# Optimization experiments

Measured on AMD Instinct MI355X. Metric: run time of the kernel, lower is better.

The kernel has to match this reference:

```python
import jax, jax.numpy as jnp
import numpy as np

B, S = 2, 2048
HID, NH, NKV, HD = 1024, 16, 4, 64
E, TOPK, INTER = 8, 2, 2816
WIN = 64
EPS = 1e-8
AUX = 0.01
NREP = NH // NKV


def _rmsnorm(x, w):
    xf = x.astype(jnp.float32)
    var = jnp.mean(xf * xf, axis=-1, keepdims=True)
    return (w * (xf * jax.lax.rsqrt(var + EPS))).astype(x.dtype)


def _rope(x, cos, sin):
    # x: [B,S,H,HD]; cos/sin: [1,S,HD//2]; matches torch view_as_complex on (..,-1,2) pairs
    xr, xi = x[..., 0::2], x[..., 1::2]
    c = cos[:, :, None, :]
    s = sin[:, :, None, :]
    return jnp.stack([xr * c - xi * s, xr * s + xi * c], axis=-1).reshape(x.shape)


def setup_inputs():
    key = jax.random.key(0)
    ks = jax.random.split(key, 12)
    sc = 0.02
    hidden_state = jax.random.normal(ks[0], (B, S, HID), jnp.float32)
    attention_mask = jnp.ones((B, S), jnp.int32)
    inv = 1.0 / (10000.0 ** (np.arange(0, HD, 2, dtype=np.float32) / HD))
    ang = np.outer(np.arange(S, dtype=np.float32), inv)
    freqs_cos = jnp.asarray(np.cos(ang), jnp.float32)[None]
    freqs_sin = jnp.asarray(np.sin(ang), jnp.float32)[None]
    wq = jax.random.normal(ks[1], (HID, NH * HD), jnp.float32) * sc
    wk = jax.random.normal(ks[2], (HID, NKV * HD), jnp.float32) * sc
    wv = jax.random.normal(ks[3], (HID, NKV * HD), jnp.float32) * sc
    wo = jax.random.normal(ks[4], (NH * HD, HID), jnp.float32) * sc
    router_w = jax.random.normal(ks[5], (HID, E), jnp.float32) * sc
    gate_w = jax.random.normal(ks[6], (E, HID, INTER), jnp.float32) * sc
    up_w = jax.random.normal(ks[7], (E, HID, INTER), jnp.float32) * sc
    down_w = jax.random.normal(ks[8], (E, INTER, HID), jnp.float32) * sc
    norm1_w = jnp.ones((HID,), jnp.float32)
    norm2_w = jnp.ones((HID,), jnp.float32)
    return dict(hidden_state=hidden_state, freqs_cos=freqs_cos, freqs_sin=freqs_sin,
                wq=wq, wk=wk, wv=wv, wo=wo, router_w=router_w,
                gate_w=gate_w, up_w=up_w, down_w=down_w,
                norm1_w=norm1_w, norm2_w=norm2_w, attention_mask=attention_mask)


def _attention(x, freqs_cos, freqs_sin, attention_mask, wq, wk, wv, wo):
    b, s, _ = x.shape
    q = (x @ wq).reshape(b, s, NH, HD)
    k = (x @ wk).reshape(b, s, NKV, HD)
    v = (x @ wv).reshape(b, s, NKV, HD)
    q = _rope(q, freqs_cos, freqs_sin)
    k = _rope(k, freqs_cos, freqs_sin)
    k = jnp.repeat(k, NREP, axis=2)  # GQA repeat_kv
    v = jnp.repeat(v, NREP, axis=2)
    scores = jnp.einsum('bqhd,bkhd->bhqk', q, k) / np.float32(np.sqrt(HD))  # [B,H,S,S]
    pos = jnp.arange(s)
    dist = pos[None, :] - pos[:, None]  # j - i
    banned = (dist > 0) | (dist < -WIN)  # causal + sliding window of 64
    scores = jnp.where(banned[None, None], -jnp.inf, scores)
    scores = jnp.where(attention_mask[:, None, None, :] == 0, -jnp.inf, scores)
    scores = jnp.maximum(scores, -1e9)  # matches clamp(min=-1e9)
    probs = jax.nn.softmax(scores.astype(jnp.float32), axis=-1).astype(q.dtype)
    probs = jnp.nan_to_num(probs)
    out = jnp.einsum('bhqk,bkhd->bqhd', probs, v).reshape(b, s, NH * HD)
    return out @ wo


def _moe(x, router_w, gate_w, up_w, down_w):
    b, s, h = x.shape
    xf = x.reshape(-1, h)  # [T, H]
    probs = jax.nn.softmax(xf @ router_w, axis=-1)  # [T, E]
    vals, idx = jax.lax.top_k(probs, TOPK)
    vals = vals / (jnp.sum(vals, axis=-1, keepdims=True) + 1e-9)
    expert_prob = jnp.mean(probs, axis=0)
    load = jnp.mean(jnp.sum(jax.nn.one_hot(idx, E, dtype=jnp.float32), axis=1), axis=0)
    router_loss = E * jnp.sum(expert_prob * load) * AUX
    out = jnp.zeros_like(xf)
    for i in range(E):  # small fixed expert loop; zero-weight tokens contribute nothing
        w_i = jnp.sum(jnp.where(idx == i, vals, 0.0), axis=-1)  # [T]
        h_i = jax.nn.silu(xf @ gate_w[i]) * (xf @ up_w[i])
        out = out + (h_i @ down_w[i]) * w_i[:, None]
    return out.reshape(b, s, h), router_loss


def reference(hidden_state, freqs_cos, freqs_sin, wq, wk, wv, wo,
              router_w, gate_w, up_w, down_w, norm1_w, norm2_w, attention_mask):
    res = hidden_state
    h = _rmsnorm(hidden_state, norm1_w)
    h = _attention(h, freqs_cos, freqs_sin, attention_mask, wq, wk, wv, wo) + res
    res = h
    h2 = _rmsnorm(h, norm2_w)
    moe_out, router_loss = _moe(h2, router_w, gate_w, up_w, down_w)
    return res + moe_out, router_loss
```

## Files before the change

kernel.cpp:

```cpp
#include <hip/hip_runtime.h>
#include <hip/hip_bf16.h>
#include <math.h>

typedef short s16x8 __attribute__((ext_vector_type(8)));
typedef float f32x4 __attribute__((ext_vector_type(4)));
typedef __hip_bfloat16 bf16;

#define NTOK 4096
#define S_LEN 2048
#define HID_C 1024
#define E_C 8
#define INTER_C 2816
#define WIN_C 64
#define CAP 4096
#define NQKV 1536
#define K2C 2048
#define ATILE 16
#define KR 80
#define OUT0_N ((size_t)NTOK*HID_C)

#define AS1 __attribute__((address_space(1)))
#define AS3 __attribute__((address_space(3)))

static __device__ __forceinline__ void gload16(const void* g, void* l){
    __builtin_amdgcn_global_load_lds((AS1 void*)(g), (AS3 void*)(l), 16, 0, 0);
}

static __device__ __forceinline__ float b2f(bf16 v){ return __bfloat162float(v); }
static __device__ __forceinline__ bf16  f2b(float v){ return __float2bfloat16(v); }
static __device__ __forceinline__ short f2bs(float v){ bf16 h = __float2bfloat16(v); return *reinterpret_cast<short*>(&h); }
struct SplitBF { short hi; short lo; };
static __device__ __forceinline__ SplitBF splitf(float x){
    SplitBF r;
    bf16 bh = __float2bfloat16(x);
    r.hi = *reinterpret_cast<short*>(&bh);
    float rem = x - __bfloat162float(bh);
    bf16 bl = __float2bfloat16(rem);
    r.lo = *reinterpret_cast<short*>(&bl);
    return r;
}


__global__ __launch_bounds__(256) void tsplit2s_k(const float* __restrict__ src,
                                                  short* __restrict__ dst,
                                                  int N, int row_off){
    __shared__ float tile[32][33];
    const int n0 = blockIdx.x*32, k0 = blockIdx.y*32;
    const int tx = threadIdx.x & 31, ty = threadIdx.x >> 5;
    #pragma unroll
    for (int i = 0; i < 4; ++i)
        tile[ty + i*8][tx] = src[(size_t)(k0 + ty + i*8)*N + n0 + tx];
    __syncthreads();
    const int g = k0 >> 5;
    const int chH = tx >> 3, chL = 4 | (tx >> 3), off = tx & 7;
    #pragma unroll
    for (int i = 0; i < 4; ++i){
        int nn = ty + i*8;
        SplitBF s = splitf(tile[tx][nn]);
        size_t rowb = (size_t)(row_off + n0 + nn)*K2C + g*64;
        dst[rowb + ((chH ^ ty)<<3) + off] = s.hi;
        dst[rowb + ((chL ^ ty)<<3) + off] = s.lo;
    }
}

__global__ __launch_bounds__(256) void tbf16s_k(const float* __restrict__ src0,
                                                short* __restrict__ dst0, int K, int N){
    const int e = blockIdx.z;
    const float* src = src0 + (size_t)e*K*N;
    short* dst = dst0 + (size_t)e*N*K;
    __shared__ float tile[32][33];
    const int n0 = blockIdx.x*32, k0 = blockIdx.y*32;
    const int tx = threadIdx.x & 31, ty = threadIdx.x >> 5;
    #pragma unroll
    for (int i = 0; i < 4; ++i)
        tile[ty + i*8][tx] = src[(size_t)(k0 + ty + i*8)*N + n0 + tx];
    __syncthreads();
    const int grp  = k0 >> 6;
    const int half = (k0 & 32) >> 3;
    const int ch   = half + (tx >> 3), off = tx & 7;
    #pragma unroll
    for (int i = 0; i < 4; ++i){
        int nn = ty + i*8;
        dst[(size_t)(n0 + nn)*K + grp*64 + ((ch ^ ty)<<3) + off] = f2bs(tile[tx][nn]);
    }
}

__global__ __launch_bounds__(256) void rmsn1c_k(const float* __restrict__ xin,
                                                const float* __restrict__ w,
                                                short* __restrict__ oc){
    const int t = blockIdx.x, tid = threadIdx.x;
    float4 v = *(const float4*)(xin + (size_t)t*HID_C + tid*4);
    float x[4] = {v.x, v.y, v.z, v.w};
    float s = x[0]*x[0]+x[1]*x[1]+x[2]*x[2]+x[3]*x[3];
    #pragma unroll
    for (int off=32; off; off>>=1) s += __shfl_xor(s, off);
    __shared__ float red[4];
    if ((tid&63)==0) red[tid>>6] = s;
    __syncthreads();
    float tot = red[0]+red[1]+red[2]+red[3];
    float sc = rsqrtf(tot*(1.0f/HID_C) + 1e-8f);
    float4 wv = *(const float4*)(w + tid*4);
    float o[4] = { x[0]*sc*wv.x, x[1]*sc*wv.y, x[2]*sc*wv.z, x[3]*sc*wv.w };
    __align__(8) short th[4], tl[4];
    #pragma unroll
    for (int i=0;i<4;++i){ SplitBF sp = splitf(o[i]); th[i]=sp.hi; tl[i]=sp.lo; }
    const int g = tid>>3, q = tid&7;
    const int ch = q>>1, sub = (q&1)*4, key = t&7;
    short* rowp = oc + (size_t)t*K2C + g*64;
    *(uint2*)(rowp + ((ch ^ key)<<3) + sub)      = *(uint2*)th;
    *(uint2*)(rowp + (((4|ch) ^ key)<<3) + sub)  = *(uint2*)tl;
}

__global__ __launch_bounds__(256) void rmsn2_k(const float* __restrict__ xin,
                                               const float* __restrict__ w,
                                               float* __restrict__ outf, bf16* __restrict__ outb){
    const int t = blockIdx.x, tid = threadIdx.x;
    float4 v = *(const float4*)(xin + (size_t)t*HID_C + tid*4);
    float x[4] = {v.x, v.y, v.z, v.w};
    float s = x[0]*x[0]+x[1]*x[1]+x[2]*x[2]+x[3]*x[3];
    #pragma unroll
    for (int off=32; off; off>>=1) s += __shfl_xor(s, off);
    __shared__ float red[4];
    if ((tid&63)==0) red[tid>>6] = s;
    __syncthreads();
    float tot = red[0]+red[1]+red[2]+red[3];
    float sc = rsqrtf(tot*(1.0f/HID_C) + 1e-8f);
    float4 wv = *(const float4*)(w + tid*4);
    float o[4] = { x[0]*sc*wv.x, x[1]*sc*wv.y, x[2]*sc*wv.z, x[3]*sc*wv.w };
    *(float4*)(outf + (size_t)t*HID_C + tid*4) = make_float4(o[0],o[1],o[2],o[3]);
    __align__(8) bf16 tmp[4] = { f2b(o[0]), f2b(o[1]), f2b(o[2]), f2b(o[3]) };
    *(uint2*)(outb + (size_t)t*HID_C + tid*4) = *(uint2*)tmp;
}

template<bool RESID>
__global__ __launch_bounds__(256) void sgemm4_k(const short* __restrict__ A2,
                                                const short* __restrict__ B2,
                                                float* __restrict__ C, const float* __restrict__ resid,
                                                int N){
    __shared__ __align__(16) short lA[2][128*64];
    __shared__ __align__(16) short lB[2][128*64];
    const int tid = threadIdx.x;
    const int bm0 = blockIdx.x*128, bn0 = blockIdx.y*128;
    const int l = tid & 63, w = tid >> 6, wr = w >> 1, wc = w & 1;
    const int lr = l >> 3, lc8 = (l & 7)*8;
    f32x4 acc[4][4] = {};
    auto STAGE = [&](int buf, int kt){
        #pragma unroll
        for (int j = 0; j < 4; ++j){
            int row = w*32 + j*8 + lr;
            gload16(A2 + (size_t)(bm0 + row)*K2C + kt*64 + lc8, &lA[buf][(w*32 + j*8)*64]);
            gload16(B2 + (size_t)(bn0 + row)*K2C + kt*64 + lc8, &lB[buf][(w*32 + j*8)*64]);
        }
    };
    STAGE(0, 0);
    for (int kt = 0; kt < 32; ++kt){
        const int cur = kt & 1;
        if (kt + 1 < 32){
            STAGE(cur ^ 1, kt + 1);
            asm volatile("s_waitcnt vmcnt(8)" ::: "memory");
        } else {
            asm volatile("s_waitcnt vmcnt(0)" ::: "memory");
        }
        __builtin_amdgcn_s_barrier();
        __builtin_amdgcn_sched_barrier(0);
        s16x8 ah[4], al[4], bh[4], bl[4];
        #pragma unroll
        for (int mi = 0; mi < 4; ++mi){
            int r = wr*64 + mi*16 + (l&15);
            int key = r & 7;
            ah[mi] = *(const s16x8*)(&lA[cur][r*64 + (((l>>4) ^ key)<<3)]);
            al[mi] = *(const s16x8*)(&lA[cur][r*64 + (((4|(l>>4)) ^ key)<<3)]);
        }
        #pragma unroll
        for (int ni = 0; ni < 4; ++ni){
            int n = wc*64 + ni*16 + (l&15);
            int key = n & 7;
            bh[ni] = *(const s16x8*)(&lB[cur][n*64 + (((l>>4) ^ key)<<3)]);
            bl[ni] = *(const s16x8*)(&lB[cur][n*64 + (((4|(l>>4)) ^ key)<<3)]);
        }
        #pragma unroll
        for (int mi = 0; mi < 4; ++mi)
            #pragma unroll
            for (int ni = 0; ni < 4; ++ni){
                acc[mi][ni] = __builtin_amdgcn_mfma_f32_16x16x32_bf16(ah[mi], bh[ni], acc[mi][ni], 0,0,0);
                acc[mi][ni] = __builtin_amdgcn_mfma_f32_16x16x32_bf16(ah[mi], bl[ni], acc[mi][ni], 0,0,0);
                acc[mi][ni] = __builtin_amdgcn_mfma_f32_16x16x32_bf16(al[mi], bh[ni], acc[mi][ni], 0,0,0);
            }
        __builtin_amdgcn_s_barrier();
    }
    #pragma unroll
    for (int mi = 0; mi < 4; ++mi)
        #pragma unroll
        for (int ni = 0; ni < 4; ++ni)
            #pragma unroll
            for (int rr = 0; rr < 4; ++rr){
                int row = bm0 + wr*64 + mi*16 + (l>>4)*4 + rr;
                int col = bn0 + wc*64 + ni*16 + (l&15);
                float vv = acc[mi][ni][rr];
                if (RESID) vv += resid[(size_t)row*N + col];
                C[(size_t)row*N + col] = vv;
            }
}

__global__ __launch_bounds__(256) void rope2_k(float* __restrict__ qkv,
                                               const float* __restrict__ cosb, const float* __restrict__ sinb){
    int idx = blockIdx.x*256 + threadIdx.x;
    int t = idx / 640;
    int r = idx - t*640;
    int hs = r >> 5, tp = r & 31;
    int s = t & (S_LEN-1);
    float c  = cosb[s*32+tp];
    float sn = sinb[s*32+tp];
    float* base;
    if (hs < 16) base = qkv + (size_t)t*NQKV + hs*64 + 2*tp;
    else         base = qkv + (size_t)t*NQKV + 1024 + (hs-16)*64 + 2*tp;
    float2 v = *(float2*)base;
    *(float2*)base = make_float2(v.x*c - v.y*sn, v.x*sn + v.y*c);
}

__global__ __launch_bounds__(256) void attn3_k(const float* __restrict__ qkv,
                                               short* __restrict__ oc){
    const int t0 = blockIdx.x * ATILE;
    const int hk = blockIdx.y;
    const int sq0 = t0 & (S_LEN-1);
    const int tokbase = t0 - sq0;
    const int tid = threadIdx.x, l = tid & 63, w = tid >> 6;
    __shared__ float Kl[KR*65];
    __shared__ float Vl[KR*65];
    __shared__ float qsh[4][64];
    __shared__ float ps[4][64];
    for (int rr = tid >> 4; rr < KR; rr += 16){
        int c4 = (tid & 15)*4;
        int kp = sq0 - 64 + rr;
        float4 kv = make_float4(0,0,0,0), vv = kv;
        if (kp >= 0){
            const float* base = qkv + (size_t)(tokbase + kp)*NQKV + 1024 + hk*64 + c4;
            kv = *(const float4*)base;
            vv = *(const float4*)(base + 256);
        }
        Kl[rr*65 + c4+0]=kv.x; Kl[rr*65 + c4+1]=kv.y; Kl[rr*65 + c4+2]=kv.z; Kl[rr*65 + c4+3]=kv.w;
        Vl[rr*65 + c4+0]=vv.x; Vl[rr*65 + c4+1]=vv.y; Vl[rr*65 + c4+2]=vv.z; Vl[rr*65 + c4+3]=vv.w;
    }
    __syncthreads();
    const int h = hk*4 + w;
    for (int i = 0; i < ATILE; ++i){
        const int t = t0 + i, sq = sq0 + i;
        qsh[w][l] = qkv[(size_t)t*NQKV + h*64 + l];
        float d = 0.f;
        const float* krow = &Kl[(i + l)*65];
        #pragma unroll
        for (int c = 0; c < 64; ++c) d += qsh[w][c] * krow[c];
        const bool valid = (sq - 64 + l) >= 0;
        float sc = valid ? d*0.125f : -1e30f;
        float part = qsh[w][l] * Kl[(i + 64)*65 + l];
        #pragma unroll
        for (int off = 32; off; off >>= 1) part += __shfl_xor(part, off);
        float dg = part*0.125f;
        float m = sc;
        #pragma unroll
        for (int off = 32; off; off >>= 1) m = fmaxf(m, __shfl_xor(m, off));
        m = fmaxf(m, dg);
        float e = __expf(sc - m);
        float ssum = e;
        #pragma unroll
        for (int off = 32; off; off >>= 1) ssum += __shfl_xor(ssum, off);
        float edg = __expf(dg - m);
        ssum += edg;
        float inv = 1.f / ssum;
        ps[w][l] = e * inv;
        float pdg = edg * inv;
        float acc = 0.f;
        #pragma unroll 8
        for (int jj = 0; jj < 64; ++jj) acc += ps[w][jj] * Vl[(i + jj)*65 + l];
        acc += pdg * Vl[(i + 64)*65 + l];
        SplitBF sp = splitf(acc);
        const int k = h*64 + l;
        const int g = k>>5, ch = (k&31)>>3, off2 = k&7, key = t&7;
        short* rowp = oc + (size_t)t*K2C + g*64;
        rowp[((ch ^ key)<<3) + off2]     = sp.hi;
        rowp[(((4|ch) ^ key)<<3) + off2] = sp.lo;
    }
}

__global__ __launch_bounds__(256) void router2_k(const float* __restrict__ h2f, const float* __restrict__ rw,
                                                 int* __restrict__ lists, float* __restrict__ wl,
                                                 int* __restrict__ cnt, float* __restrict__ psum){
    const int tid = threadIdx.x, l = tid & 63, w = tid >> 6;
    __shared__ int   sE0[16], sE1[16], sSlot0[16], sSlot1[16];
    __shared__ float sW0[16], sW1[16];
    __shared__ float sPsum[8];
    __shared__ int   sCnt[8], sBase[8];
    if (tid < 8){ sPsum[tid] = 0.f; sCnt[tid] = 0; }
    __syncthreads();
    #pragma unroll
    for (int i = 0; i < 4; ++i){
        const int li = w*4 + i;
        const int t = blockIdx.x*16 + li;
        float lg[8] = {0,0,0,0,0,0,0,0};
        for (int c = 0; c < 16; ++c){
            int kidx = l + c*64;
            float x = h2f[(size_t)t*HID_C + kidx];
            float4 w0 = *(const float4*)(rw + (size_t)kidx*8);
            float4 w1 = *(const float4*)(rw + (size_t)kidx*8 + 4);
            lg[0] += x*w0.x; lg[1] += x*w0.y; lg[2] += x*w0.z; lg[3] += x*w0.w;
            lg[4] += x*w1.x; lg[5] += x*w1.y; lg[6] += x*w1.z; lg[7] += x*w1.w;
        }
        #pragma unroll
        for (int e = 0; e < 8; ++e)
            #pragma unroll
            for (int off=32; off; off>>=1) lg[e] += __shfl_xor(lg[e], off);
        if (l == 0){
            float m = lg[0];
            #pragma unroll
            for (int e = 1; e < 8; ++e) m = fmaxf(m, lg[e]);
            float p[8]; float s = 0.f;
            #pragma unroll
            for (int e = 0; e < 8; ++e){ p[e] = __expf(lg[e]-m); s += p[e]; }
            float invs = 1.f/s;
            #pragma unroll
            for (int e = 0; e < 8; ++e){ p[e] *= invs; atomicAdd(&sPsum[e], p[e]); }
            float best = -1e30f, sec = -1e30f; int bi = 0, si = 0;
            #pragma unroll
            for (int e = 0; e < 8; ++e){
                float pv = p[e];
                if (pv > best){ sec = best; si = bi; best = pv; bi = e; }
                else if (pv > sec){ sec = pv; si = e; }
            }
            float wsum = best + sec + 1e-9f;
            sE0[li] = bi; sE1[li] = si;
            sW0[li] = best/wsum; sW1[li] = sec/wsum;
            sSlot0[li] = atomicAdd(&sCnt[bi], 1);
            sSlot1[li] = atomicAdd(&sCnt[si], 1);
        }
    }
    __syncthreads();
    if (tid < 8){
        sBase[tid] = atomicAdd(&cnt[tid], sCnt[tid]);
        atomicAdd(&psum[tid], sPsum[tid]);
    }
    __syncthreads();
    if (tid < 16){
        int t = blockIdx.x*16 + tid;
        int e0 = sE0[tid], e1 = sE1[tid];
        int s0 = sBase[e0] + sSlot0[tid];
        int s1 = sBase[e1] + sSlot1[tid];
        lists[e0*CAP + s0] = t; wl[e0*CAP + s0] = sW0[tid];
        lists[e1*CAP + s1] = t; wl[e1*CAP + s1] = sW1[tid];
    }
}

__global__ void finalize_k(const int* __restrict__ cnt, const float* __restrict__ psum,
                           int* __restrict__ offs, float* __restrict__ out){
    if (threadIdx.x == 0 && blockIdx.x == 0){
        int o = 0; float loss = 0.f;
        for (int e = 0; e < 8; ++e){
            offs[e] = o; o += cnt[e];
            loss += (psum[e]*(1.0f/NTOK)) * ((float)cnt[e]*(1.0f/NTOK));
        }
        offs[8] = o;
        out[OUT0_N] = loss * (float)E_C * 0.01f;
    }
}

__global__ __launch_bounds__(256) void moe1g3_k(const short* __restrict__ h2b,
                                                const short* __restrict__ gate_t,
                                                const short* __restrict__ up_t,
                                                bf16* __restrict__ inter,
                                                const int* __restrict__ lists,
                                                const int* __restrict__ cnt,
                                                const int* __restrict__ offs){
    const int b = blockIdx.x;
    const int r = b & 7, j = b >> 3;
    const int G = r + ((j >> 5) << 3);
    const int e = G / 44, bnG = G % 44;
    const int bm0 = (j & 31) * 128;
    const int ne = cnt[e];
    if (bm0 >= ne) return;
    const int bn0 = bnG * 64;
    __shared__ __align__(16) short lA[2][128*64];
    __shared__ __align__(16) short lG[2][64*64];
    __shared__ __align__(16) short lU[2][64*64];
    const int tid = threadIdx.x;
    const int l = tid & 63, w = tid >> 6, wr = w >> 1, wc = w & 1;
    const int lr = l >> 3, lc8 = (l & 7)*8;
    const int lcs = (((l & 7) ^ lr) << 3);
    const short* Gb = gate_t + (size_t)e*INTER_C*HID_C;
    const short* Ub = up_t   + (size_t)e*INTER_C*HID_C;
    int tokA[4];
    #pragma unroll
    for (int jj = 0; jj < 4; ++jj){
        int slot = bm0 + w*32 + jj*8 + lr;
        if (slot >= ne) slot = ne - 1;
        tokA[jj] = lists[e*CAP + slot];
    }
    auto STAGE = [&](int buf, int kt){
        #pragma unroll
        for (int jj = 0; jj < 4; ++jj)
            gload16(h2b + (size_t)tokA[jj]*HID_C + kt*64 + lcs, &lA[buf][(w*32 + jj*8)*64]);
        #pragma unroll
        for (int jj = 0; jj < 2; ++jj){
            int n = w*16 + jj*8 + lr;
            gload16(Gb + (size_t)(bn0 + n)*HID_C + kt*64 + lc8, &lG[buf][(w*16 + jj*8)*64]);
            gload16(Ub + (size_t)(bn0 + n)*HID_C + kt*64 + lc8, &lU[buf][(w*16 + jj*8)*64]);
        }
    };
    f32x4 ag[4][2] = {}; f32x4 au[4][2] = {};
    STAGE(0, 0);
    for (int kt = 0; kt < 16; ++kt){
        const int cur = kt & 1;
        if (kt + 1 < 16){
            STAGE(cur ^ 1, kt + 1);
            asm volatile("s_waitcnt vmcnt(8)" ::: "memory");
        } else {
            asm volatile("s_waitcnt vmcnt(0)" ::: "memory");
        }
        __builtin_amdgcn_s_barrier();
        __builtin_amdgcn_sched_barrier(0);
        __builtin_amdgcn_s_setprio(1);
        #pragma unroll
        for (int kk = 0; kk < 64; kk += 32){
            s16x8 af[4], bg[2], bu[2];
            #pragma unroll
            for (int mi = 0; mi < 4; ++mi){
                int ra = wr*64 + mi*16 + (l&15);
                int keyA = ra & 7;
                int chA = (kk>>3) + (l>>4);
                af[mi] = *(const s16x8*)(&lA[cur][ra*64 + ((chA ^ keyA)<<3)]);
            }
            #pragma unroll
            for (int ni = 0; ni < 2; ++ni){
                int n = wc*32 + ni*16 + (l&15);
                int key = n & 7;
                int ch = (kk>>3) + (l>>4);
                bg[ni] = *(const s16x8*)(&lG[cur][n*64 + ((ch ^ key)<<3)]);
                bu[ni] = *(const s16x8*)(&lU[cur][n*64 + ((ch ^ key)<<3)]);
            }
            #pragma unroll
            for (int mi = 0; mi < 4; ++mi)
                #pragma unroll
                for (int ni = 0; ni < 2; ++ni){
                    ag[mi][ni] = __builtin_amdgcn_mfma_f32_16x16x32_bf16(af[mi], bg[ni], ag[mi][ni], 0,0,0);
                    au[mi][ni] = __builtin_amdgcn_mfma_f32_16x16x32_bf16(af[mi], bu[ni], au[mi][ni], 0,0,0);
                }
        }
        __builtin_amdgcn_s_setprio(0);
        __builtin_amdgcn_s_barrier();
    }
    const int obase = offs[e];
    #pragma unroll
    for (int mi = 0; mi < 4; ++mi)
        #pragma unroll
        for (int ni = 0; ni < 2; ++ni)
            #pragma unroll
            for (int rr = 0; rr < 4; ++rr){
                int slot = bm0 + wr*64 + mi*16 + (l>>4)*4 + rr;
                if (slot < ne){
                    int col = bn0 + wc*32 + ni*16 + (l&15);
                    float g = ag[mi][ni][rr], uu = au[mi][ni][rr];
                    float val = (g/(1.f+__expf(-g)))*uu;
                    inter[(size_t)(obase+slot)*INTER_C + col] = f2b(val);
                }
            }
}

__global__ __launch_bounds__(256) void moe2g3_k(const bf16* __restrict__ inter,
                                                const short* __restrict__ down_t,
                                                float* __restrict__ outp,
                                                const float* __restrict__ wl,
                                                const int* __restrict__ lists,
                                                const int* __restrict__ cnt,
                                                const int* __restrict__ offs){
    const int b = blockIdx.x;
    const int r = b & 7, j = b >> 3;
    const int G = r + ((j >> 5) << 3);
    const int e = G >> 3, bnG = G & 7;
    const int bm0 = (j & 31) * 128;
    const int ne = cnt[e];
    if (bm0 >= ne) return;
    const int bn0 = bnG * 128;
    __shared__ __align__(16) short lA[2][128*64];
    __shared__ __align__(16) short lB[2][128*64];
    const int tid = threadIdx.x;
    const int l = tid & 63, w = tid >> 6, wr = w >> 1, wc = w & 1;
    const int lr = l >> 3, lc8 = (l & 7)*8;
    const int lcs = (((l & 7) ^ lr) << 3);
    const int obase = offs[e];
    const short* Db = down_t + (size_t)e*HID_C*INTER_C;
    const short* As = (const short*)inter;
    int rowA[4];
    #pragma unroll
    for (int jj = 0; jj < 4; ++jj){
        int slot = bm0 + w*32 + jj*8 + lr;
        if (slot >= ne) slot = ne - 1;
        rowA[jj] = obase + slot;
    }
    auto STAGE = [&](int buf, int kt){
        #pragma unroll
        for (int jj = 0; jj < 4; ++jj){
            gload16(As + (size_t)rowA[jj]*INTER_C + kt*64 + lcs, &lA[buf][(w*32 + jj*8)*64]);
            int n = w*32 + jj*8 + lr;
            gload16(Db + (size_t)(bn0 + n)*INTER_C + kt*64 + lc8, &lB[buf][(w*32 + jj*8)*64]);
        }
    };
    f32x4 acc[4][4] = {};
    STAGE(0, 0);
    for (int kt = 0; kt < 44; ++kt){
        const int cur = kt & 1;
        if (kt + 1 < 44){
            STAGE(cur ^ 1, kt + 1);
            asm volatile("s_waitcnt vmcnt(8)" ::: "memory");
        } else {
            asm volatile("s_waitcnt vmcnt(0)" ::: "memory");
        }
        __builtin_amdgcn_s_barrier();
        __builtin_amdgcn_sched_barrier(0);
        __builtin_amdgcn_s_setprio(1);
        #pragma unroll
        for (int kk = 0; kk < 64; kk += 32){
            s16x8 af[4], bfr[4];
            #pragma unroll
            for (int mi = 0; mi < 4; ++mi){
                int ra = wr*64 + mi*16 + (l&15);
                int keyA = ra & 7;
                int chA = (kk>>3) + (l>>4);
                af[mi] = *(const s16x8*)(&lA[cur][ra*64 + ((chA ^ keyA)<<3)]);
            }
            #pragma unroll
            for (int ni = 0; ni < 4; ++ni){
                int n = wc*64 + ni*16 + (l&15);
                int key = n & 7;
                int ch = (kk>>3) + (l>>4);
                bfr[ni] = *(const s16x8*)(&lB[cur][n*64 + ((ch ^ key)<<3)]);
            }
            #pragma unroll
            for (int mi = 0; mi < 4; ++mi)
                #pragma unroll
                for (int ni = 0; ni < 4; ++ni)
                    acc[mi][ni] = __builtin_amdgcn_mfma_f32_16x16x32_bf16(af[mi], bfr[ni], acc[mi][ni], 0,0,0);
        }
        __builtin_amdgcn_s_setprio(0);
        __builtin_amdgcn_s_barrier();
    }
    #pragma unroll
    for (int mi = 0; mi < 4; ++mi)
        #pragma unroll
        for (int ni = 0; ni < 4; ++ni)
            #pragma unroll
            for (int rr = 0; rr < 4; ++rr){
                int slot = bm0 + wr*64 + mi*16 + (l>>4)*4 + rr;
                if (slot < ne){
                    int col = bn0 + wc*64 + ni*16 + (l&15);
                    int tok = lists[e*CAP + slot];
                    float wgt = wl[e*CAP + slot];
                    atomicAdd(&outp[(size_t)tok*HID_C + col], acc[mi][ni][rr]*wgt);
                }
            }
}

__global__ __launch_bounds__(256) void final_k(const float* __restrict__ hres,
                                               float* __restrict__ out){
    const int t = blockIdx.x, c = threadIdx.x*4;
    float4 hv = *(const float4*)(hres + (size_t)t*HID_C + c);
    *(float4*)(out + (size_t)t*HID_C + c) = hv;
}

extern "C" void kernel_launch(void* const* d_in, const int* in_sizes, int n_in,
                              void* d_out, int out_size, void* d_ws, size_t ws_size,
                              hipStream_t stream){
    const float* hidden  = (const float*)d_in[0];
    const float* fcos    = (const float*)d_in[1];
    const float* fsin    = (const float*)d_in[2];
    const float* wq      = (const float*)d_in[3];
    const float* wk      = (const float*)d_in[4];
    const float* wv      = (const float*)d_in[5];
    const float* wo      = (const float*)d_in[6];
    const float* routerw = (const float*)d_in[7];
    const float* gatew   = (const float*)d_in[8];
    const float* upw     = (const float*)d_in[9];
    const float* downw   = (const float*)d_in[10];
    const float* n1w     = (const float*)d_in[11];
    const float* n2w     = (const float*)d_in[12];

    char* p = (char*)d_ws;
    size_t off = 0;
    auto alloc = [&](size_t b)->void*{ void* r = p + off; off = (off + b + 255) & ~(size_t)255; return r; };

    int*   cnt    = (int*)alloc(64);
    float* psum   = (float*)alloc(64);
    int*   offs   = (int*)alloc(64);
    int*   lists  = (int*)alloc((size_t)E_C*CAP*4);
    float* wl     = (float*)alloc((size_t)E_C*CAP*4);
    short* wqkv2  = (short*)alloc((size_t)NQKV*K2C*2);
    short* wo2    = (short*)alloc((size_t)HID_C*K2C*2);
    short* gate_t = (short*)alloc((size_t)E_C*INTER_C*HID_C*2);
    short* up_t   = (short*)alloc((size_t)E_C*INTER_C*HID_C*2);
    short* down_t = (short*)alloc((size_t)E_C*HID_C*INTER_C*2);
    short* h1c    = (short*)alloc((size_t)NTOK*K2C*2);
    float* qkvf   = (float*)alloc((size_t)NTOK*NQKV*4);
    float* hres   = (float*)alloc((size_t)NTOK*HID_C*4);
    bf16*  inter  = (bf16*)alloc((size_t)2*NTOK*INTER_C*2);

    short* oc  = h1c;
    float* h2f = qkvf;
    bf16*  h2b = (bf16*)(qkvf + (size_t)NTOK*HID_C);
    float* outp = (float*)d_out;

    (void)hipMemsetAsync(cnt, 0, 64, stream);
    (void)hipMemsetAsync(psum, 0, 64, stream);

    tsplit2s_k<<<dim3(32,32), 256, 0, stream>>>(wq, wqkv2, 1024, 0);
    tsplit2s_k<<<dim3(8,32),  256, 0, stream>>>(wk, wqkv2, 256, 1024);
    tsplit2s_k<<<dim3(8,32),  256, 0, stream>>>(wv, wqkv2, 256, 1280);
    tsplit2s_k<<<dim3(32,32), 256, 0, stream>>>(wo, wo2, 1024, 0);
    tbf16s_k<<<dim3(88,32,8), 256, 0, stream>>>(gatew, gate_t, 1024, 2816);
    tbf16s_k<<<dim3(88,32,8), 256, 0, stream>>>(upw,   up_t,   1024, 2816);
    tbf16s_k<<<dim3(32,88,8), 256, 0, stream>>>(downw, down_t, 2816, 1024);

    rmsn1c_k<<<NTOK, 256, 0, stream>>>(hidden, n1w, h1c);
    sgemm4_k<false><<<dim3(32,12), 256, 0, stream>>>(h1c, wqkv2, qkvf, nullptr, NQKV);
    rope2_k<<<10240, 256, 0, stream>>>(qkvf, fcos, fsin);
    attn3_k<<<dim3(NTOK/ATILE, 4), 256, 0, stream>>>(qkvf, oc);
    sgemm4_k<true><<<dim3(32,8), 256, 0, stream>>>(oc, wo2, hres, hidden, 1024);
    rmsn2_k<<<NTOK, 256, 0, stream>>>(hres, n2w, h2f, h2b);
    router2_k<<<256, 256, 0, stream>>>(h2f, routerw, lists, wl, cnt, psum);
    finalize_k<<<1, 64, 0, stream>>>(cnt, psum, offs, outp);
    final_k<<<NTOK, 256, 0, stream>>>(hres, outp);
    moe1g3_k<<<11264, 256, 0, stream>>>((const short*)h2b, gate_t, up_t, inter, lists, cnt, offs);
    moe2g3_k<<<2048, 256, 0, stream>>>(inter, down_t, outp, wl, lists, cnt, offs);
}
```

Measured before the change: 684.6 us.

## Load MoE weight fragments directly from global into registers, bypassing LDS

Both MoE GEMM kernels now read the B-operand (gate/up and down weights) straight from global memory into MFMA register fragments each k-step, instead of staging them through shared memory. Only the token activations stay double-buffered in LDS. The aim is to cut LDS traffic and footprint, which could raise occupancy and remove LDS reads for B. In exchange, the weight loads are less coalesced (each lane fetches 16 bytes from a different row), they are issued without prefetch ahead of the current step, and tiles shared across waves are fetched redundantly. The vmcnt wait counts are adjusted to match the new number of outstanding loads.

```diff
diff --git a/kernel.cpp b/kernel.cpp
--- a/kernel.cpp
+++ b/kernel.cpp
@@ -362,7 +362,7 @@
     }
 }
 
-__global__ __launch_bounds__(256) void moe1g3_k(const short* __restrict__ h2b,
+__global__ __launch_bounds__(256) void moe1g4_k(const short* __restrict__ h2b,
                                                 const short* __restrict__ gate_t,
                                                 const short* __restrict__ up_t,
                                                 bf16* __restrict__ inter,
@@ -378,11 +378,9 @@
     if (bm0 >= ne) return;
     const int bn0 = bnG * 64;
     __shared__ __align__(16) short lA[2][128*64];
-    __shared__ __align__(16) short lG[2][64*64];
-    __shared__ __align__(16) short lU[2][64*64];
     const int tid = threadIdx.x;
     const int l = tid & 63, w = tid >> 6, wr = w >> 1, wc = w & 1;
-    const int lr = l >> 3, lc8 = (l & 7)*8;
+    const int lr = l >> 3;
     const int lcs = (((l & 7) ^ lr) << 3);
     const short* Gb = gate_t + (size_t)e*INTER_C*HID_C;
     const short* Ub = up_t   + (size_t)e*INTER_C*HID_C;
@@ -393,54 +391,57 @@
         if (slot >= ne) slot = ne - 1;
         tokA[jj] = lists[e*CAP + slot];
     }
+    size_t bOffs[2][2];
+    #pragma unroll
+    for (int kki = 0; kki < 2; ++kki)
+        #pragma unroll
+        for (int ni = 0; ni < 2; ++ni){
+            int n = wc*32 + ni*16 + (l&15);
+            int ch = kki*4 + (l>>4);
+            bOffs[kki][ni] = (size_t)(bn0 + n)*HID_C + (((ch ^ (n&7)))<<3);
+        }
     auto STAGE = [&](int buf, int kt){
         #pragma unroll
         for (int jj = 0; jj < 4; ++jj)
             gload16(h2b + (size_t)tokA[jj]*HID_C + kt*64 + lcs, &lA[buf][(w*32 + jj*8)*64]);
-        #pragma unroll
-        for (int jj = 0; jj < 2; ++jj){
-            int n = w*16 + jj*8 + lr;
-            gload16(Gb + (size_t)(bn0 + n)*HID_C + kt*64 + lc8, &lG[buf][(w*16 + jj*8)*64]);
-            gload16(Ub + (size_t)(bn0 + n)*HID_C + kt*64 + lc8, &lU[buf][(w*16 + jj*8)*64]);
-        }
     };
     f32x4 ag[4][2] = {}; f32x4 au[4][2] = {};
     STAGE(0, 0);
     for (int kt = 0; kt < 16; ++kt){
         const int cur = kt & 1;
+        s16x8 bgv[2][2], buv[2][2];
+        #pragma unroll
+        for (int kki = 0; kki < 2; ++kki)
+            #pragma unroll
+            for (int ni = 0; ni < 2; ++ni){
+                bgv[kki][ni] = *(const s16x8*)(Gb + bOffs[kki][ni] + kt*64);
+                buv[kki][ni] = *(const s16x8*)(Ub + bOffs[kki][ni] + kt*64);
+            }
         if (kt + 1 < 16){
             STAGE(cur ^ 1, kt + 1);
+            asm volatile("s_waitcnt vmcnt(12)" ::: "memory");
+        } else {
             asm volatile("s_waitcnt vmcnt(8)" ::: "memory");
-        } else {
-            asm volatile("s_waitcnt vmcnt(0)" ::: "memory");
         }
         __builtin_amdgcn_s_barrier();
         __builtin_amdgcn_sched_barrier(0);
         __builtin_amdgcn_s_setprio(1);
         #pragma unroll
-        for (int kk = 0; kk < 64; kk += 32){
-            s16x8 af[4], bg[2], bu[2];
+        for (int kki = 0; kki < 2; ++kki){
+            const int kk = kki*32;
+            s16x8 af[4];
             #pragma unroll
             for (int mi = 0; mi < 4; ++mi){
                 int ra = wr*64 + mi*16 + (l&15);
-                int keyA = ra & 7;
                 int chA = (kk>>3) + (l>>4);
-                af[mi] = *(const s16x8*)(&lA[cur][ra*64 + ((chA ^ keyA)<<3)]);
-            }
-            #pragma unroll
-            for (int ni = 0; ni < 2; ++ni){
-                int n = wc*32 + ni*16 + (l&15);
-                int key = n & 7;
-                int ch = (kk>>3) + (l>>4);
-                bg[ni] = *(const s16x8*)(&lG[cur][n*64 + ((ch ^ key)<<3)]);
-                bu[ni] = *(const s16x8*)(&lU[cur][n*64 + ((ch ^ key)<<3)]);
+                af[mi] = *(const s16x8*)(&lA[cur][ra*64 + ((chA ^ (ra&7))<<3)]);
             }
             #pragma unroll
             for (int mi = 0; mi < 4; ++mi)
                 #pragma unroll
                 for (int ni = 0; ni < 2; ++ni){
-                    ag[mi][ni] = __builtin_amdgcn_mfma_f32_16x16x32_bf16(af[mi], bg[ni], ag[mi][ni], 0,0,0);
-                    au[mi][ni] = __builtin_amdgcn_mfma_f32_16x16x32_bf16(af[mi], bu[ni], au[mi][ni], 0,0,0);
+                    ag[mi][ni] = __builtin_amdgcn_mfma_f32_16x16x32_bf16(af[mi], bgv[kki][ni], ag[mi][ni], 0,0,0);
+                    au[mi][ni] = __builtin_amdgcn_mfma_f32_16x16x32_bf16(af[mi], buv[kki][ni], au[mi][ni], 0,0,0);
                 }
         }
         __builtin_amdgcn_s_setprio(0);
@@ -463,7 +464,7 @@
             }
 }
 
-__global__ __launch_bounds__(256) void moe2g3_k(const bf16* __restrict__ inter,
+__global__ __launch_bounds__(256) void moe2g4_k(const bf16* __restrict__ inter,
                                                 const short* __restrict__ down_t,
                                                 float* __restrict__ outp,
                                                 const float* __restrict__ wl,
@@ -479,10 +480,9 @@
     if (bm0 >= ne) return;
     const int bn0 = bnG * 128;
     __shared__ __align__(16) short lA[2][128*64];
-    __shared__ __align__(16) short lB[2][128*64];
     const int tid = threadIdx.x;
     const int l = tid & 63, w = tid >> 6, wr = w >> 1, wc = w & 1;
-    const int lr = l >> 3, lc8 = (l & 7)*8;
+    const int lr = l >> 3;
     const int lcs = (((l & 7) ^ lr) << 3);
     const int obase = offs[e];
     const short* Db = down_t + (size_t)e*HID_C*INTER_C;
@@ -494,49 +494,54 @@
         if (slot >= ne) slot = ne - 1;
         rowA[jj] = obase + slot;
     }
+    size_t bOffs[2][4];
+    #pragma unroll
+    for (int kki = 0; kki < 2; ++kki)
+        #pragma unroll
+        for (int ni = 0; ni < 4; ++ni){
+            int n = wc*64 + ni*16 + (l&15);
+            int ch = kki*4 + (l>>4);
+            bOffs[kki][ni] = (size_t)(bn0 + n)*INTER_C + (((ch ^ (n&7)))<<3);
+        }
     auto STAGE = [&](int buf, int kt){
         #pragma unroll
-        for (int jj = 0; jj < 4; ++jj){
+        for (int jj = 0; jj < 4; ++jj)
             gload16(As + (size_t)rowA[jj]*INTER_C + kt*64 + lcs, &lA[buf][(w*32 + jj*8)*64]);
-            int n = w*32 + jj*8 + lr;
-            gload16(Db + (size_t)(bn0 + n)*INTER_C + kt*64 + lc8, &lB[buf][(w*32 + jj*8)*64]);
-        }
     };
     f32x4 acc[4][4] = {};
     STAGE(0, 0);
     for (int kt = 0; kt < 44; ++kt){
         const int cur = kt & 1;
+        s16x8 bfv[2][4];
+        #pragma unroll
+        for (int kki = 0; kki < 2; ++kki)
+            #pragma unroll
+            for (int ni = 0; ni < 4; ++ni)
+                bfv[kki][ni] = *(const s16x8*)(Db + bOffs[kki][ni] + kt*64);
         if (kt + 1 < 44){
             STAGE(cur ^ 1, kt + 1);
+            asm volatile("s_waitcnt vmcnt(12)" ::: "memory");
+        } else {
             asm volatile("s_waitcnt vmcnt(8)" ::: "memory");
-        } else {
-            asm volatile("s_waitcnt vmcnt(0)" ::: "memory");
         }
         __builtin_amdgcn_s_barrier();
         __builtin_amdgcn_sched_barrier(0);
         __builtin_amdgcn_s_setprio(1);
         #pragma unroll
-        for (int kk = 0; kk < 64; kk += 32){
-            s16x8 af[4], bfr[4];
+        for (int kki = 0; kki < 2; ++kki){
+            const int kk = kki*32;
+            s16x8 af[4];
             #pragma unroll
             for (int mi = 0; mi < 4; ++mi){
                 int ra = wr*64 + mi*16 + (l&15);
-                int keyA = ra & 7;
                 int chA = (kk>>3) + (l>>4);
-                af[mi] = *(const s16x8*)(&lA[cur][ra*64 + ((chA ^ keyA)<<3)]);
-            }
-            #pragma unroll
-            for (int ni = 0; ni < 4; ++ni){
-                int n = wc*64 + ni*16 + (l&15);
-                int key = n & 7;
-                int ch = (kk>>3) + (l>>4);
-                bfr[ni] = *(const s16x8*)(&lB[cur][n*64 + ((ch ^ key)<<3)]);
+                af[mi] = *(const s16x8*)(&lA[cur][ra*64 + ((chA ^ (ra&7))<<3)]);
             }
             #pragma unroll
             for (int mi = 0; mi < 4; ++mi)
                 #pragma unroll
                 for (int ni = 0; ni < 4; ++ni)
-                    acc[mi][ni] = __builtin_amdgcn_mfma_f32_16x16x32_bf16(af[mi], bfr[ni], acc[mi][ni], 0,0,0);
+                    acc[mi][ni] = __builtin_amdgcn_mfma_f32_16x16x32_bf16(af[mi], bfv[kki][ni], acc[mi][ni], 0,0,0);
         }
         __builtin_amdgcn_s_setprio(0);
         __builtin_amdgcn_s_barrier();
@@ -625,6 +630,6 @@
     router2_k<<<256, 256, 0, stream>>>(h2f, routerw, lists, wl, cnt, psum);
     finalize_k<<<1, 64, 0, stream>>>(cnt, psum, offs, outp);
     final_k<<<NTOK, 256, 0, stream>>>(hres, outp);
-    moe1g3_k<<<11264, 256, 0, stream>>>((const short*)h2b, gate_t, up_t, inter, lists, cnt, offs);
-    moe2g3_k<<<2048, 256, 0, stream>>>(inter, down_t, outp, wl, lists, cnt, offs);
-}
+    moe1g4_k<<<11264, 256, 0, stream>>>((const short*)h2b, gate_t, up_t, inter, lists, cnt, offs);
+    moe2g4_k<<<2048, 256, 0, stream>>>(inter, down_t, outp, wl, lists, cnt, offs);
+}
```

Measured after the change: 717.7 us. 1.05x slower.
